# Kernel tuning notes

Hardware: AMD Instinct MI355X
Metric: run time of the kernel (lower is better)

## Reference

```python
import jax, jax.numpy as jnp
import numpy as np

N = 50000      # nodes
E = 800000     # edges (avg degree 16)
D_IN = 128
D_H = 128
D_OUT = 64


def setup_inputs() -> dict:
    key = jax.random.key(0)
    k_x, k_e, k_w1, k_b1, k_w2, k_b2 = jax.random.split(key, 6)
    x = jax.random.normal(k_x, (N, D_IN), dtype=jnp.float32)
    edge_index = jax.random.randint(k_e, (2, E), 0, N, dtype=jnp.int32)
    # Glorot-style init for GCN weights, zero bias (as in PyG GCNConv defaults)
    W1 = jax.random.normal(k_w1, (D_IN, D_H), dtype=jnp.float32) * (1.0 / np.sqrt(D_IN))
    b1 = jnp.zeros((D_H,), dtype=jnp.float32)
    W2 = jax.random.normal(k_w2, (D_H, D_OUT), dtype=jnp.float32) * (1.0 / np.sqrt(D_H))
    b2 = jnp.zeros((D_OUT,), dtype=jnp.float32)
    return {"x": x, "edge_index": edge_index, "W1": W1, "b1": b1, "W2": W2, "b2": b2}


def _gcn_norm(edge_index, n):
    # PyG gcn_norm with add_self_loops=True, edge_weight = 1
    loops = jnp.arange(n, dtype=edge_index.dtype)
    src = jnp.concatenate([edge_index[0], loops])  # [E+N]
    dst = jnp.concatenate([edge_index[1], loops])
    deg = jax.ops.segment_sum(jnp.ones_like(dst, dtype=jnp.float32), dst, num_segments=n)
    dinv = jnp.where(deg > 0, jax.lax.rsqrt(deg), 0.0)
    norm = dinv[src] * dinv[dst]                   # [E+N]
    return src, dst, norm


def _gcn_conv(h, src, dst, norm, W, b, n):
    # transform -> gather source -> scale by symmetric norm -> scatter-add at dst -> bias
    hW = h @ W                                      # [N, F_out]
    msg = hW[src] * norm[:, None]                   # [E+N, F_out]
    agg = jax.ops.segment_sum(msg, dst, num_segments=n)
    return agg + b


def reference(x, edge_index, W1, b1, W2, b2):
    n = x.shape[0]
    src, dst, norm = _gcn_norm(edge_index, n)
    x1 = jax.nn.relu(_gcn_conv(x, src, dst, norm, W1, b1, n))
    x2 = _gcn_conv(x1, src, dst, norm, W2, b2, n)
    return x2
```

## Files before the change

kernel.cpp:

```cpp
#include <hip/hip_runtime.h>

#define CAP  64
#define BN   64
#define NBMAX 1024
#define ECAP 2048
#define P1E  4096

typedef unsigned int uint;
typedef unsigned short ushort;
typedef __attribute__((ext_vector_type(8))) short short8;
typedef __attribute__((ext_vector_type(4))) float f32x4;

__device__ inline ushort f2bf(float f) {
    uint u = __float_as_uint(f);
    return (ushort)((u + 0x7fffu + ((u >> 16) & 1u)) >> 16);
}
__device__ inline uint packbf2(float lo, float hi) {
    return (uint)f2bf(lo) | ((uint)f2bf(hi) << 16);
}
__device__ inline void unpackbf2(uint u, float& lo, float& hi) {
    lo = __uint_as_float(u << 16);
    hi = __uint_as_float(u & 0xffff0000u);
}

__global__ __launch_bounds__(256) void k_init(const float* __restrict__ W1,
                                              const float* __restrict__ W2,
                                              ushort* __restrict__ W1t,
                                              ushort* __restrict__ W2t,
                                              int* __restrict__ gtail) {
    int i = blockIdx.x * 256 + threadIdx.x;
    if (i < NBMAX) gtail[i] = 0;
    if (i < 4 * 128 * 32) {
        int kt = i >> 12;
        int nn = (i >> 5) & 127;
        int ko = i & 31;
        W1t[i] = f2bf(W1[(size_t)(kt * 32 + ko) * 128 + nn]);
    }
    int j = i - 4 * 128 * 32;
    if (j >= 0 && j < 4 * 64 * 32) {
        int kt = j >> 11;
        int nn = (j >> 5) & 63;
        int ko = j & 31;
        W2t[j] = f2bf(W2[(size_t)(kt * 32 + ko) * 64 + nn]);
    }
}

__global__ __launch_bounds__(256) void k_part(const int* __restrict__ esrc,
                                              const int* __restrict__ edst,
                                              int E, int nb,
                                              int* __restrict__ gtail,
                                              uint* __restrict__ ebuf) {
    __shared__ int hist[NBMAX];
    int base_e = blockIdx.x * P1E;
    for (int i = threadIdx.x; i < nb; i += 256) hist[i] = 0;
    __syncthreads();

    int d[16], s[16];
#pragma unroll
    for (int u = 0; u < 16; u++) {
        int e = base_e + u * 256 + threadIdx.x;
        d[u] = (e < E) ? edst[e] : -1;
        s[u] = (e < E) ? esrc[e] : 0;
        if (d[u] >= 0) atomicAdd(&hist[d[u] >> 6], 1);
    }
    __syncthreads();

    for (int i = threadIdx.x; i < nb; i += 256) {
        int h = hist[i];
        hist[i] = (h > 0) ? atomicAdd(&gtail[i], h) : 0;
    }
    __syncthreads();

#pragma unroll
    for (int u = 0; u < 16; u++) {
        if (d[u] >= 0) {
            int b = d[u] >> 6;
            int slot = atomicAdd(&hist[b], 1);
            if (slot < ECAP)
                ebuf[(size_t)b * ECAP + slot] =
                    ((uint)(d[u] & (BN - 1)) << 16) | (uint)s[u];
        }
    }
}

__global__ __launch_bounds__(256) void k_csr(const uint* __restrict__ ebuf,
                                             const int* __restrict__ gtail,
                                             int n,
                                             ushort* __restrict__ colbuf,
                                             int* __restrict__ cnt,
                                             float* __restrict__ dinv) {
    __shared__ ushort cb[BN * CAP];
    __shared__ int cl[BN];
    int b = blockIdx.x;
    int ne = gtail[b];
    if (ne > ECAP) ne = ECAP;
    for (int i = threadIdx.x; i < BN; i += 256) cl[i] = 0;
    __syncthreads();

    const uint* eb = ebuf + (size_t)b * ECAP;
    for (int i = threadIdx.x; i < ne; i += 256) {
        uint pr = eb[i];
        int dloc = pr >> 16;
        int p = atomicAdd(&cl[dloc], 1);
        if (p < CAP) cb[dloc * CAP + p] = (ushort)(pr & 0xffffu);
    }
    __syncthreads();

    int node0 = b * BN;
    for (int i = threadIdx.x; i < BN * CAP / 8; i += 256) {
        int node = node0 + i / (CAP / 8);
        if (node < n)
            ((uint4*)&colbuf[(size_t)node0 * CAP])[i] = ((const uint4*)cb)[i];
    }
    for (int i = threadIdx.x; i < BN; i += 256) {
        int node = node0 + i;
        if (node < n) {
            int c = cl[i];
            dinv[node] = rsqrtf((float)c + 1.0f);
            cnt[node] = (c > CAP) ? CAP : c;
        }
    }
}

__global__ __launch_bounds__(256) void k_mgemm1(const float* __restrict__ Xf,
                                                const ushort* __restrict__ Wt,
                                                ushort* __restrict__ Yb, int n) {
    __shared__ ushort Ws[4 * 128 * 32];
    for (int idx = threadIdx.x; idx < 4 * 128 * 32 / 8; idx += 256)
        ((uint4*)Ws)[idx] = ((const uint4*)Wt)[idx];
    __syncthreads();

    int wid  = threadIdx.x >> 6;
    int l    = threadIdx.x & 63;
    int mrow = l & 15;
    int kgrp = l >> 4;
    int row16 = (blockIdx.x * 4 + wid) * 16;
    int r  = row16 + mrow;
    int rc = (r < n) ? r : (n - 1);

    f32x4 acc[8];
#pragma unroll
    for (int t = 0; t < 8; t++) acc[t] = (f32x4){0.f, 0.f, 0.f, 0.f};

#pragma unroll
    for (int kt = 0; kt < 4; kt++) {
        const float* xp = &Xf[(size_t)rc * 128 + kt * 32 + kgrp * 8];
        float4 x0 = *(const float4*)xp;
        float4 x1 = *(const float4*)(xp + 4);
        short8 a;
        a[0] = (short)f2bf(x0.x); a[1] = (short)f2bf(x0.y);
        a[2] = (short)f2bf(x0.z); a[3] = (short)f2bf(x0.w);
        a[4] = (short)f2bf(x1.x); a[5] = (short)f2bf(x1.y);
        a[6] = (short)f2bf(x1.z); a[7] = (short)f2bf(x1.w);
#pragma unroll
        for (int t = 0; t < 8; t++) {
            short8 b = *(const short8*)&Ws[((kt * 128) + t * 16 + mrow) * 32 + kgrp * 8];
            acc[t] = __builtin_amdgcn_mfma_f32_16x16x32_bf16(a, b, acc[t], 0, 0, 0);
        }
    }

    int orow = row16 + kgrp * 4;
#pragma unroll
    for (int t = 0; t < 8; t++) {
#pragma unroll
        for (int q = 0; q < 4; q++) {
            int rr = orow + q;
            if (rr < n) Yb[(size_t)rr * 128 + t * 16 + mrow] = f2bf(acc[t][q]);
        }
    }
}

__global__ __launch_bounds__(256) void k_mgemm2(const ushort* __restrict__ Xh,
                                                const ushort* __restrict__ Wt,
                                                ushort* __restrict__ Yb, int n) {
    __shared__ ushort Ws[4 * 64 * 32];
    for (int idx = threadIdx.x; idx < 4 * 64 * 32 / 8; idx += 256)
        ((uint4*)Ws)[idx] = ((const uint4*)Wt)[idx];
    __syncthreads();

    int wid  = threadIdx.x >> 6;
    int l    = threadIdx.x & 63;
    int mrow = l & 15;
    int kgrp = l >> 4;
    int row16 = (blockIdx.x * 4 + wid) * 16;
    int r  = row16 + mrow;
    int rc = (r < n) ? r : (n - 1);

    f32x4 acc[4];
#pragma unroll
    for (int t = 0; t < 4; t++) acc[t] = (f32x4){0.f, 0.f, 0.f, 0.f};

#pragma unroll
    for (int kt = 0; kt < 4; kt++) {
        short8 a = *(const short8*)&Xh[(size_t)rc * 128 + kt * 32 + kgrp * 8];
#pragma unroll
        for (int t = 0; t < 4; t++) {
            short8 b = *(const short8*)&Ws[((kt * 64) + t * 16 + mrow) * 32 + kgrp * 8];
            acc[t] = __builtin_amdgcn_mfma_f32_16x16x32_bf16(a, b, acc[t], 0, 0, 0);
        }
    }

    int orow = row16 + kgrp * 4;
#pragma unroll
    for (int t = 0; t < 4; t++) {
#pragma unroll
        for (int q = 0; q < 4; q++) {
            int rr = orow + q;
            if (rr < n) Yb[(size_t)rr * 64 + t * 16 + mrow] = f2bf(acc[t][q]);
        }
    }
}

__global__ __launch_bounds__(256) void k_agg1(const ushort* __restrict__ Hb,
                                              const int* __restrict__ cntc,
                                              const ushort* __restrict__ colbuf,
                                              const float* __restrict__ dinv,
                                              const float* __restrict__ b1,
                                              ushort* __restrict__ x1b, int n) {
    const int CH = 128, LPG = 16;
    int t    = blockIdx.x * 256 + threadIdx.x;
    int gid  = t / LPG;
    int lane = t % LPG;
    if (gid >= n) return;

    float di = dinv[gid];
    int c = cntc[gid];
    if (c > CAP) c = CAP;

    uint4 aself = *(const uint4*)(Hb + (size_t)gid * CH + lane * 8);
    float4 bb0 = *(const float4*)&b1[lane * 8];
    float4 bb1 = *(const float4*)&b1[lane * 8 + 4];

    float acc[8];
#pragma unroll
    for (int k = 0; k < 8; k++) acc[k] = 0.f;

    const ushort* cb = colbuf + (size_t)gid * CAP;
    for (int j = 0; j < c; j += 16) {
        uint4 iv0 = *(const uint4*)(cb + j);
        uint4 iv1 = *(const uint4*)(cb + j + 8);
        uint ivw[8] = {iv0.x, iv0.y, iv0.z, iv0.w, iv1.x, iv1.y, iv1.z, iv1.w};
        int s[16];
#pragma unroll
        for (int u = 0; u < 8; u++) {
            s[2 * u]     = ivw[u] & 0xffff;
            s[2 * u + 1] = ivw[u] >> 16;
        }
#pragma unroll
        for (int u = 1; u < 16; u++) if (j + u >= c) s[u] = s[0];
        float w[16];
#pragma unroll
        for (int u = 0; u < 16; u++)
            w[u] = (j + u < c) ? dinv[s[u]] : 0.f;
        uint4 h[16];
#pragma unroll
        for (int u = 0; u < 16; u++)
            h[u] = *(const uint4*)(Hb + (size_t)s[u] * CH + lane * 8);
#pragma unroll
        for (int u = 0; u < 16; u++) {
            float f0, f1;
            unpackbf2(h[u].x, f0, f1); acc[0] += f0 * w[u]; acc[1] += f1 * w[u];
            unpackbf2(h[u].y, f0, f1); acc[2] += f0 * w[u]; acc[3] += f1 * w[u];
            unpackbf2(h[u].z, f0, f1); acc[4] += f0 * w[u]; acc[5] += f1 * w[u];
            unpackbf2(h[u].w, f0, f1); acc[6] += f0 * w[u]; acc[7] += f1 * w[u];
        }
    }

    float sf[8];
    unpackbf2(aself.x, sf[0], sf[1]);
    unpackbf2(aself.y, sf[2], sf[3]);
    unpackbf2(aself.z, sf[4], sf[5]);
    unpackbf2(aself.w, sf[6], sf[7]);
    float bb[8] = {bb0.x, bb0.y, bb0.z, bb0.w, bb1.x, bb1.y, bb1.z, bb1.w};

    float xv[8];
#pragma unroll
    for (int k = 0; k < 8; k++)
        xv[k] = fmaxf((acc[k] + di * sf[k]) * di + bb[k], 0.f);

    uint up[4] = { packbf2(xv[0], xv[1]), packbf2(xv[2], xv[3]),
                   packbf2(xv[4], xv[5]), packbf2(xv[6], xv[7]) };
    *(uint4*)&x1b[(size_t)gid * CH + lane * 8] = *(uint4*)up;
}

__global__ __launch_bounds__(256) void k_agg2(const ushort* __restrict__ Hb,
                                              const int* __restrict__ cntc,
                                              const ushort* __restrict__ colbuf,
                                              const float* __restrict__ dinv,
                                              const float* __restrict__ b2,
                                              float* __restrict__ out, int n) {
    const int CH = 64, LPG = 8;
    int t    = blockIdx.x * 256 + threadIdx.x;
    int gid  = t / LPG;
    int lane = t % LPG;
    if (gid >= n) return;

    float di = dinv[gid];
    int c = cntc[gid];
    if (c > CAP) c = CAP;

    uint4 aself = *(const uint4*)(Hb + (size_t)gid * CH + lane * 8);
    float4 bb0 = *(const float4*)&b2[lane * 8];
    float4 bb1 = *(const float4*)&b2[lane * 8 + 4];

    float acc[8];
#pragma unroll
    for (int k = 0; k < 8; k++) acc[k] = 0.f;

    const ushort* cb = colbuf + (size_t)gid * CAP;
    for (int j = 0; j < c; j += 16) {
        uint4 iv0 = *(const uint4*)(cb + j);
        uint4 iv1 = *(const uint4*)(cb + j + 8);
        uint ivw[8] = {iv0.x, iv0.y, iv0.z, iv0.w, iv1.x, iv1.y, iv1.z, iv1.w};
        int s[16];
#pragma unroll
        for (int u = 0; u < 8; u++) {
            s[2 * u]     = ivw[u] & 0xffff;
            s[2 * u + 1] = ivw[u] >> 16;
        }
#pragma unroll
        for (int u = 1; u < 16; u++) if (j + u >= c) s[u] = s[0];
        float w[16];
#pragma unroll
        for (int u = 0; u < 16; u++)
            w[u] = (j + u < c) ? dinv[s[u]] : 0.f;
        uint4 h[16];
#pragma unroll
        for (int u = 0; u < 16; u++)
            h[u] = *(const uint4*)(Hb + (size_t)s[u] * CH + lane * 8);
#pragma unroll
        for (int u = 0; u < 16; u++) {
            float f0, f1;
            unpackbf2(h[u].x, f0, f1); acc[0] += f0 * w[u]; acc[1] += f1 * w[u];
            unpackbf2(h[u].y, f0, f1); acc[2] += f0 * w[u]; acc[3] += f1 * w[u];
            unpackbf2(h[u].z, f0, f1); acc[4] += f0 * w[u]; acc[5] += f1 * w[u];
            unpackbf2(h[u].w, f0, f1); acc[6] += f0 * w[u]; acc[7] += f1 * w[u];
        }
    }

    float sf[8];
    unpackbf2(aself.x, sf[0], sf[1]);
    unpackbf2(aself.y, sf[2], sf[3]);
    unpackbf2(aself.z, sf[4], sf[5]);
    unpackbf2(aself.w, sf[6], sf[7]);
    float bb[8] = {bb0.x, bb0.y, bb0.z, bb0.w, bb1.x, bb1.y, bb1.z, bb1.w};

    float o[8];
#pragma unroll
    for (int k = 0; k < 8; k++)
        o[k] = (acc[k] + di * sf[k]) * di + bb[k];

    float* dst = out + (size_t)gid * CH + lane * 8;
    *(float4*)dst       = make_float4(o[0], o[1], o[2], o[3]);
    *(float4*)(dst + 4) = make_float4(o[4], o[5], o[6], o[7]);
}

extern "C" void kernel_launch(void* const* d_in, const int* in_sizes, int n_in,
                              void* d_out, int out_size, void* d_ws, size_t ws_size,
                              hipStream_t stream) {
    const float* x  = (const float*)d_in[0];
    const int*   ei = (const int*)d_in[1];
    const float* W1 = (const float*)d_in[2];
    const float* b1 = (const float*)d_in[3];
    const float* W2 = (const float*)d_in[4];
    const float* b2 = (const float*)d_in[5];
    float* out = (float*)d_out;

    int N = in_sizes[0] / 128;
    int E = in_sizes[1] / 2;
    const int* esrc = ei;
    const int* edst = ei + E;

    int nb = (N + BN - 1) / BN;

    char* ws = (char*)d_ws;
    size_t off = 0;
    auto alloc = [&](size_t bytes) -> void* {
        off = (off + 255) & ~(size_t)255;
        void* p = ws + off;
        off += bytes;
        return p;
    };
    int*    gtail   = (int*)   alloc((size_t)NBMAX * 4);
    int*    cnt     = (int*)   alloc((size_t)N * 4);
    float*  dinv    = (float*) alloc((size_t)N * 4);
    uint*   ebuf    = (uint*)  alloc((size_t)nb * ECAP * 4);
    ushort* colbuf  = (ushort*)alloc((size_t)nb * BN * CAP * 2 + 256);
    ushort* hW1b    = (ushort*)alloc((size_t)N * 128 * 2);
    ushort* x1b     = (ushort*)alloc((size_t)N * 128 * 2);
    ushort* hW2b    = (ushort*)alloc((size_t)N * 64 * 2);
    ushort* W1t     = (ushort*)alloc((size_t)4 * 128 * 32 * 2);
    ushort* W2t     = (ushort*)alloc((size_t)4 * 64 * 32 * 2);

    k_init<<<96, 256, 0, stream>>>(W1, W2, W1t, W2t, gtail);

    int nbP1 = (E + P1E - 1) / P1E;
    k_part<<<nbP1, 256, 0, stream>>>(esrc, edst, E, nb, gtail, ebuf);
    k_mgemm1<<<(N + 63) / 64, 256, 0, stream>>>(x, W1t, hW1b, N);
    k_csr<<<nb, 256, 0, stream>>>(ebuf, gtail, N, colbuf, cnt, dinv);

    k_agg1<<<((size_t)N * 16 + 255) / 256, 256, 0, stream>>>(
        hW1b, cnt, colbuf, dinv, b1, x1b, N);

    k_mgemm2<<<(N + 63) / 64, 256, 0, stream>>>(x1b, W2t, hW2b, N);

    k_agg2<<<((size_t)N * 8 + 255) / 256, 256, 0, stream>>>(
        hW2b, cnt, colbuf, dinv, b2, out, N);
}
```

Measured before the change: 93.86 us.

## Process two nodes per lane group in aggregation and vectorize edge loads

Each aggregation lane group now handles two destination nodes instead of one. The first index chunk, self row and degree values for both nodes are loaded up front, so their latency overlaps with the first node's gather. The grid is halved to match. Edge partition and CSR build kernels switch from scalar to int4/uint4 loads. This trades parallelism (half as many threads) and higher register pressure for more memory-level parallelism per thread and fewer load instructions.

```diff
diff --git a/kernel.cpp b/kernel.cpp
--- a/kernel.cpp
+++ b/kernel.cpp
@@ -22,6 +22,28 @@
     lo = __uint_as_float(u << 16);
     hi = __uint_as_float(u & 0xffff0000u);
 }
+
+#define UNPACK16(s, v0, v1)                                        \
+    {   uint _w[8] = {v0.x, v0.y, v0.z, v0.w, v1.x, v1.y, v1.z, v1.w}; \
+        _Pragma("unroll")                                          \
+        for (int _u = 0; _u < 8; _u++) {                           \
+            s[2*_u]   = _w[_u] & 0xffff;                           \
+            s[2*_u+1] = _w[_u] >> 16;                              \
+        } }
+
+#define GATHER16(acc, s, w, Hb, CH, lane)                          \
+    {   uint4 _h[16];                                              \
+        _Pragma("unroll")                                          \
+        for (int _u = 0; _u < 16; _u++)                            \
+            _h[_u] = *(const uint4*)((Hb) + (size_t)(s)[_u] * (CH) + (lane) * 8); \
+        _Pragma("unroll")                                          \
+        for (int _u = 0; _u < 16; _u++) {                          \
+            float _f0, _f1;                                        \
+            unpackbf2(_h[_u].x, _f0, _f1); acc[0] += _f0 * (w)[_u]; acc[1] += _f1 * (w)[_u]; \
+            unpackbf2(_h[_u].y, _f0, _f1); acc[2] += _f0 * (w)[_u]; acc[3] += _f1 * (w)[_u]; \
+            unpackbf2(_h[_u].z, _f0, _f1); acc[4] += _f0 * (w)[_u]; acc[5] += _f1 * (w)[_u]; \
+            unpackbf2(_h[_u].w, _f0, _f1); acc[6] += _f0 * (w)[_u]; acc[7] += _f1 * (w)[_u]; \
+        } }
 
 __global__ __launch_bounds__(256) void k_init(const float* __restrict__ W1,
                                               const float* __restrict__ W2,
@@ -51,18 +73,34 @@
                                               int* __restrict__ gtail,
                                               uint* __restrict__ ebuf) {
     __shared__ int hist[NBMAX];
-    int base_e = blockIdx.x * P1E;
+    int base = blockIdx.x * P1E;
     for (int i = threadIdx.x; i < nb; i += 256) hist[i] = 0;
     __syncthreads();
 
     int d[16], s[16];
 #pragma unroll
-    for (int u = 0; u < 16; u++) {
-        int e = base_e + u * 256 + threadIdx.x;
-        d[u] = (e < E) ? edst[e] : -1;
-        s[u] = (e < E) ? esrc[e] : 0;
+    for (int u = 0; u < 4; u++) {
+        int e = base + (u * 256 + threadIdx.x) * 4;
+        int4 dd, ss;
+        if (e + 3 < E) {
+            dd = *(const int4*)(edst + e);
+            ss = *(const int4*)(esrc + e);
+        } else {
+            dd.x = (e     < E) ? edst[e]     : -1;
+            dd.y = (e + 1 < E) ? edst[e + 1] : -1;
+            dd.z = (e + 2 < E) ? edst[e + 2] : -1;
+            dd.w = (e + 3 < E) ? edst[e + 3] : -1;
+            ss.x = (e     < E) ? esrc[e]     : 0;
+            ss.y = (e + 1 < E) ? esrc[e + 1] : 0;
+            ss.z = (e + 2 < E) ? esrc[e + 2] : 0;
+            ss.w = (e + 3 < E) ? esrc[e + 3] : 0;
+        }
+        d[4*u] = dd.x; d[4*u+1] = dd.y; d[4*u+2] = dd.z; d[4*u+3] = dd.w;
+        s[4*u] = ss.x; s[4*u+1] = ss.y; s[4*u+2] = ss.z; s[4*u+3] = ss.w;
+    }
+#pragma unroll
+    for (int u = 0; u < 16; u++)
         if (d[u] >= 0) atomicAdd(&hist[d[u] >> 6], 1);
-    }
     __syncthreads();
 
     for (int i = threadIdx.x; i < nb; i += 256) {
@@ -98,11 +136,17 @@
     __syncthreads();
 
     const uint* eb = ebuf + (size_t)b * ECAP;
-    for (int i = threadIdx.x; i < ne; i += 256) {
-        uint pr = eb[i];
-        int dloc = pr >> 16;
-        int p = atomicAdd(&cl[dloc], 1);
-        if (p < CAP) cb[dloc * CAP + p] = (ushort)(pr & 0xffffu);
+    for (int i = threadIdx.x * 4; i < ne; i += 1024) {
+        uint4 pr4 = *(const uint4*)(eb + i);
+        uint prs[4] = {pr4.x, pr4.y, pr4.z, pr4.w};
+#pragma unroll
+        for (int k = 0; k < 4; k++) {
+            if (i + k < ne) {
+                int dloc = prs[k] >> 16;
+                int p = atomicAdd(&cl[dloc], 1);
+                if (p < CAP) cb[dloc * CAP + p] = (ushort)(prs[k] & 0xffffu);
+            }
+        }
     }
     __syncthreads();
 
@@ -219,68 +263,104 @@
                                               ushort* __restrict__ x1b, int n) {
     const int CH = 128, LPG = 16;
     int t    = blockIdx.x * 256 + threadIdx.x;
-    int gid  = t / LPG;
+    int g    = t / LPG;
     int lane = t % LPG;
-    if (gid >= n) return;
-
-    float di = dinv[gid];
-    int c = cntc[gid];
-    if (c > CAP) c = CAP;
-
-    uint4 aself = *(const uint4*)(Hb + (size_t)gid * CH + lane * 8);
-    float4 bb0 = *(const float4*)&b1[lane * 8];
-    float4 bb1 = *(const float4*)&b1[lane * 8 + 4];
+    int g0   = g * 2;
+    if (g0 >= n) return;
+    int g1   = g0 + 1;
+    bool has1 = (g1 < n);
+    int gc1  = has1 ? g1 : g0;
+
+    float di0 = dinv[g0], di1 = dinv[gc1];
+    int c0 = cntc[g0];  if (c0 > CAP) c0 = CAP;
+    int c1 = has1 ? cntc[g1] : 0;  if (c1 > CAP) c1 = CAP;
+    const ushort* cb0 = colbuf + (size_t)g0  * CAP;
+    const ushort* cb1 = colbuf + (size_t)gc1 * CAP;
+    uint4 iva0 = *(const uint4*)(cb0);
+    uint4 iva1 = *(const uint4*)(cb0 + 8);
+    uint4 ivb0 = *(const uint4*)(cb1);
+    uint4 ivb1 = *(const uint4*)(cb1 + 8);
+    uint4 self0 = *(const uint4*)(Hb + (size_t)g0  * CH + lane * 8);
+    uint4 self1 = *(const uint4*)(Hb + (size_t)gc1 * CH + lane * 8);
+    float4 bbl = *(const float4*)&b1[lane * 8];
+    float4 bbh = *(const float4*)&b1[lane * 8 + 4];
+    float bb[8] = {bbl.x, bbl.y, bbl.z, bbl.w, bbh.x, bbh.y, bbh.z, bbh.w};
 
     float acc[8];
 #pragma unroll
     for (int k = 0; k < 8; k++) acc[k] = 0.f;
-
-    const ushort* cb = colbuf + (size_t)gid * CAP;
-    for (int j = 0; j < c; j += 16) {
-        uint4 iv0 = *(const uint4*)(cb + j);
-        uint4 iv1 = *(const uint4*)(cb + j + 8);
-        uint ivw[8] = {iv0.x, iv0.y, iv0.z, iv0.w, iv1.x, iv1.y, iv1.z, iv1.w};
+    {
         int s[16];
-#pragma unroll
-        for (int u = 0; u < 8; u++) {
-            s[2 * u]     = ivw[u] & 0xffff;
-            s[2 * u + 1] = ivw[u] >> 16;
-        }
-#pragma unroll
-        for (int u = 1; u < 16; u++) if (j + u >= c) s[u] = s[0];
+        UNPACK16(s, iva0, iva1);
+#pragma unroll
+        for (int u = 1; u < 16; u++) if (u >= c0) s[u] = s[0];
         float w[16];
 #pragma unroll
-        for (int u = 0; u < 16; u++)
-            w[u] = (j + u < c) ? dinv[s[u]] : 0.f;
-        uint4 h[16];
-#pragma unroll
-        for (int u = 0; u < 16; u++)
-            h[u] = *(const uint4*)(Hb + (size_t)s[u] * CH + lane * 8);
-#pragma unroll
-        for (int u = 0; u < 16; u++) {
-            float f0, f1;
-            unpackbf2(h[u].x, f0, f1); acc[0] += f0 * w[u]; acc[1] += f1 * w[u];
-            unpackbf2(h[u].y, f0, f1); acc[2] += f0 * w[u]; acc[3] += f1 * w[u];
-            unpackbf2(h[u].z, f0, f1); acc[4] += f0 * w[u]; acc[5] += f1 * w[u];
-            unpackbf2(h[u].w, f0, f1); acc[6] += f0 * w[u]; acc[7] += f1 * w[u];
-        }
-    }
-
-    float sf[8];
-    unpackbf2(aself.x, sf[0], sf[1]);
-    unpackbf2(aself.y, sf[2], sf[3]);
-    unpackbf2(aself.z, sf[4], sf[5]);
-    unpackbf2(aself.w, sf[6], sf[7]);
-    float bb[8] = {bb0.x, bb0.y, bb0.z, bb0.w, bb1.x, bb1.y, bb1.z, bb1.w};
-
-    float xv[8];
-#pragma unroll
-    for (int k = 0; k < 8; k++)
-        xv[k] = fmaxf((acc[k] + di * sf[k]) * di + bb[k], 0.f);
-
-    uint up[4] = { packbf2(xv[0], xv[1]), packbf2(xv[2], xv[3]),
-                   packbf2(xv[4], xv[5]), packbf2(xv[6], xv[7]) };
-    *(uint4*)&x1b[(size_t)gid * CH + lane * 8] = *(uint4*)up;
+        for (int u = 0; u < 16; u++) w[u] = (u < c0) ? dinv[s[u]] : 0.f;
+        if (c0 > 0) GATHER16(acc, s, w, Hb, CH, lane);
+        for (int j = 16; j < c0; j += 16) {
+            uint4 v0 = *(const uint4*)(cb0 + j);
+            uint4 v1 = *(const uint4*)(cb0 + j + 8);
+            UNPACK16(s, v0, v1);
+#pragma unroll
+            for (int u = 1; u < 16; u++) if (j + u >= c0) s[u] = s[0];
+#pragma unroll
+            for (int u = 0; u < 16; u++) w[u] = (j + u < c0) ? dinv[s[u]] : 0.f;
+            GATHER16(acc, s, w, Hb, CH, lane);
+        }
+    }
+    {
+        float sf[8];
+        unpackbf2(self0.x, sf[0], sf[1]);
+        unpackbf2(self0.y, sf[2], sf[3]);
+        unpackbf2(self0.z, sf[4], sf[5]);
+        unpackbf2(self0.w, sf[6], sf[7]);
+        float xv[8];
+#pragma unroll
+        for (int k = 0; k < 8; k++)
+            xv[k] = fmaxf((acc[k] + di0 * sf[k]) * di0 + bb[k], 0.f);
+        uint up[4] = { packbf2(xv[0], xv[1]), packbf2(xv[2], xv[3]),
+                       packbf2(xv[4], xv[5]), packbf2(xv[6], xv[7]) };
+        *(uint4*)&x1b[(size_t)g0 * CH + lane * 8] = *(uint4*)up;
+    }
+
+    if (!has1) return;
+#pragma unroll
+    for (int k = 0; k < 8; k++) acc[k] = 0.f;
+    {
+        int s[16];
+        UNPACK16(s, ivb0, ivb1);
+#pragma unroll
+        for (int u = 1; u < 16; u++) if (u >= c1) s[u] = s[0];
+        float w[16];
+#pragma unroll
+        for (int u = 0; u < 16; u++) w[u] = (u < c1) ? dinv[s[u]] : 0.f;
+        if (c1 > 0) GATHER16(acc, s, w, Hb, CH, lane);
+        for (int j = 16; j < c1; j += 16) {
+            uint4 v0 = *(const uint4*)(cb1 + j);
+            uint4 v1 = *(const uint4*)(cb1 + j + 8);
+            UNPACK16(s, v0, v1);
+#pragma unroll
+            for (int u = 1; u < 16; u++) if (j + u >= c1) s[u] = s[0];
+#pragma unroll
+            for (int u = 0; u < 16; u++) w[u] = (j + u < c1) ? dinv[s[u]] : 0.f;
+            GATHER16(acc, s, w, Hb, CH, lane);
+        }
+    }
+    {
+        float sf[8];
+        unpackbf2(self1.x, sf[0], sf[1]);
+        unpackbf2(self1.y, sf[2], sf[3]);
+        unpackbf2(self1.z, sf[4], sf[5]);
+        unpackbf2(self1.w, sf[6], sf[7]);
+        float xv[8];
+#pragma unroll
+        for (int k = 0; k < 8; k++)
+            xv[k] = fmaxf((acc[k] + di1 * sf[k]) * di1 + bb[k], 0.f);
+        uint up[4] = { packbf2(xv[0], xv[1]), packbf2(xv[2], xv[3]),
+                       packbf2(xv[4], xv[5]), packbf2(xv[6], xv[7]) };
+        *(uint4*)&x1b[(size_t)g1 * CH + lane * 8] = *(uint4*)up;
+    }
 }
 
 __global__ __launch_bounds__(256) void k_agg2(const ushort* __restrict__ Hb,
@@ -291,68 +371,104 @@
                                               float* __restrict__ out, int n) {
     const int CH = 64, LPG = 8;
     int t    = blockIdx.x * 256 + threadIdx.x;
-    int gid  = t / LPG;
+    int g    = t / LPG;
     int lane = t % LPG;
-    if (gid >= n) return;
-
-    float di = dinv[gid];
-    int c = cntc[gid];
-    if (c > CAP) c = CAP;
-
-    uint4 aself = *(const uint4*)(Hb + (size_t)gid * CH + lane * 8);
-    float4 bb0 = *(const float4*)&b2[lane * 8];
-    float4 bb1 = *(const float4*)&b2[lane * 8 + 4];
+    int g0   = g * 2;
+    if (g0 >= n) return;
+    int g1   = g0 + 1;
+    bool has1 = (g1 < n);
+    int gc1  = has1 ? g1 : g0;
+
+    float di0 = dinv[g0], di1 = dinv[gc1];
+    int c0 = cntc[g0];  if (c0 > CAP) c0 = CAP;
+    int c1 = has1 ? cntc[g1] : 0;  if (c1 > CAP) c1 = CAP;
+    const ushort* cb0 = colbuf + (size_t)g0  * CAP;
+    const ushort* cb1 = colbuf + (size_t)gc1 * CAP;
+    uint4 iva0 = *(const uint4*)(cb0);
+    uint4 iva1 = *(const uint4*)(cb0 + 8);
+    uint4 ivb0 = *(const uint4*)(cb1);
+    uint4 ivb1 = *(const uint4*)(cb1 + 8);
+    uint4 self0 = *(const uint4*)(Hb + (size_t)g0  * CH + lane * 8);
+    uint4 self1 = *(const uint4*)(Hb + (size_t)gc1 * CH + lane * 8);
+    float4 bbl = *(const float4*)&b2[lane * 8];
+    float4 bbh = *(const float4*)&b2[lane * 8 + 4];
+    float bb[8] = {bbl.x, bbl.y, bbl.z, bbl.w, bbh.x, bbh.y, bbh.z, bbh.w};
 
     float acc[8];
 #pragma unroll
     for (int k = 0; k < 8; k++) acc[k] = 0.f;
-
-    const ushort* cb = colbuf + (size_t)gid * CAP;
-    for (int j = 0; j < c; j += 16) {
-        uint4 iv0 = *(const uint4*)(cb + j);
-        uint4 iv1 = *(const uint4*)(cb + j + 8);
-        uint ivw[8] = {iv0.x, iv0.y, iv0.z, iv0.w, iv1.x, iv1.y, iv1.z, iv1.w};
+    {
         int s[16];
-#pragma unroll
-        for (int u = 0; u < 8; u++) {
-            s[2 * u]     = ivw[u] & 0xffff;
-            s[2 * u + 1] = ivw[u] >> 16;
-        }
-#pragma unroll
-        for (int u = 1; u < 16; u++) if (j + u >= c) s[u] = s[0];
+        UNPACK16(s, iva0, iva1);
+#pragma unroll
+        for (int u = 1; u < 16; u++) if (u >= c0) s[u] = s[0];
         float w[16];
 #pragma unroll
-        for (int u = 0; u < 16; u++)
-            w[u] = (j + u < c) ? dinv[s[u]] : 0.f;
-        uint4 h[16];
-#pragma unroll
-        for (int u = 0; u < 16; u++)
-            h[u] = *(const uint4*)(Hb + (size_t)s[u] * CH + lane * 8);
-#pragma unroll
-        for (int u = 0; u < 16; u++) {
-            float f0, f1;
-            unpackbf2(h[u].x, f0, f1); acc[0] += f0 * w[u]; acc[1] += f1 * w[u];
-            unpackbf2(h[u].y, f0, f1); acc[2] += f0 * w[u]; acc[3] += f1 * w[u];
-            unpackbf2(h[u].z, f0, f1); acc[4] += f0 * w[u]; acc[5] += f1 * w[u];
-            unpackbf2(h[u].w, f0, f1); acc[6] += f0 * w[u]; acc[7] += f1 * w[u];
-        }
-    }
-
-    float sf[8];
-    unpackbf2(aself.x, sf[0], sf[1]);
-    unpackbf2(aself.y, sf[2], sf[3]);
-    unpackbf2(aself.z, sf[4], sf[5]);
-    unpackbf2(aself.w, sf[6], sf[7]);
-    float bb[8] = {bb0.x, bb0.y, bb0.z, bb0.w, bb1.x, bb1.y, bb1.z, bb1.w};
-
-    float o[8];
-#pragma unroll
-    for (int k = 0; k < 8; k++)
-        o[k] = (acc[k] + di * sf[k]) * di + bb[k];
-
-    float* dst = out + (size_t)gid * CH + lane * 8;
-    *(float4*)dst       = make_float4(o[0], o[1], o[2], o[3]);
-    *(float4*)(dst + 4) = make_float4(o[4], o[5], o[6], o[7]);
+        for (int u = 0; u < 16; u++) w[u] = (u < c0) ? dinv[s[u]] : 0.f;
+        if (c0 > 0) GATHER16(acc, s, w, Hb, CH, lane);
+        for (int j = 16; j < c0; j += 16) {
+            uint4 v0 = *(const uint4*)(cb0 + j);
+            uint4 v1 = *(const uint4*)(cb0 + j + 8);
+            UNPACK16(s, v0, v1);
+#pragma unroll
+            for (int u = 1; u < 16; u++) if (j + u >= c0) s[u] = s[0];
+#pragma unroll
+            for (int u = 0; u < 16; u++) w[u] = (j + u < c0) ? dinv[s[u]] : 0.f;
+            GATHER16(acc, s, w, Hb, CH, lane);
+        }
+    }
+    {
+        float sf[8];
+        unpackbf2(self0.x, sf[0], sf[1]);
+        unpackbf2(self0.y, sf[2], sf[3]);
+        unpackbf2(self0.z, sf[4], sf[5]);
+        unpackbf2(self0.w, sf[6], sf[7]);
+        float o[8];
+#pragma unroll
+        for (int k = 0; k < 8; k++)
+            o[k] = (acc[k] + di0 * sf[k]) * di0 + bb[k];
+        float* dst = out + (size_t)g0 * CH + lane * 8;
+        *(float4*)dst       = make_float4(o[0], o[1], o[2], o[3]);
+        *(float4*)(dst + 4) = make_float4(o[4], o[5], o[6], o[7]);
+    }
+
+    if (!has1) return;
+#pragma unroll
+    for (int k = 0; k < 8; k++) acc[k] = 0.f;
+    {
+        int s[16];
+        UNPACK16(s, ivb0, ivb1);
+#pragma unroll
+        for (int u = 1; u < 16; u++) if (u >= c1) s[u] = s[0];
+        float w[16];
+#pragma unroll
+        for (int u = 0; u < 16; u++) w[u] = (u < c1) ? dinv[s[u]] : 0.f;
+        if (c1 > 0) GATHER16(acc, s, w, Hb, CH, lane);
+        for (int j = 16; j < c1; j += 16) {
+            uint4 v0 = *(const uint4*)(cb1 + j);
+            uint4 v1 = *(const uint4*)(cb1 + j + 8);
+            UNPACK16(s, v0, v1);
+#pragma unroll
+            for (int u = 1; u < 16; u++) if (j + u >= c1) s[u] = s[0];
+#pragma unroll
+            for (int u = 0; u < 16; u++) w[u] = (j + u < c1) ? dinv[s[u]] : 0.f;
+            GATHER16(acc, s, w, Hb, CH, lane);
+        }
+    }
+    {
+        float sf[8];
+        unpackbf2(self1.x, sf[0], sf[1]);
+        unpackbf2(self1.y, sf[2], sf[3]);
+        unpackbf2(self1.z, sf[4], sf[5]);
+        unpackbf2(self1.w, sf[6], sf[7]);
+        float o[8];
+#pragma unroll
+        for (int k = 0; k < 8; k++)
+            o[k] = (acc[k] + di1 * sf[k]) * di1 + bb[k];
+        float* dst = out + (size_t)g1 * CH + lane * 8;
+        *(float4*)dst       = make_float4(o[0], o[1], o[2], o[3]);
+        *(float4*)(dst + 4) = make_float4(o[4], o[5], o[6], o[7]);
+    }
 }
 
 extern "C" void kernel_launch(void* const* d_in, const int* in_sizes, int n_in,
@@ -399,11 +515,12 @@
     k_mgemm1<<<(N + 63) / 64, 256, 0, stream>>>(x, W1t, hW1b, N);
     k_csr<<<nb, 256, 0, stream>>>(ebuf, gtail, N, colbuf, cnt, dinv);
 
-    k_agg1<<<((size_t)N * 16 + 255) / 256, 256, 0, stream>>>(
+    int ng1 = (N + 1) / 2;
+    k_agg1<<<((size_t)ng1 * 16 + 255) / 256, 256, 0, stream>>>(
         hW1b, cnt, colbuf, dinv, b1, x1b, N);
 
     k_mgemm2<<<(N + 63) / 64, 256, 0, stream>>>(x1b, W2t, hW2b, N);
 
-    k_agg2<<<((size_t)N * 8 + 255) / 256, 256, 0, stream>>>(
+    k_agg2<<<((size_t)ng1 * 8 + 255) / 256, 256, 0, stream>>>(
         hW2b, cnt, colbuf, dinv, b2, out, N);
 }
```

Measured after the change: 97.45 us. 1.04x slower.
